# Optimization experiments

Measured on AMD Instinct MI355X. Metric: run time of the kernel, lower is better.

## Reference

```python
import jax, jax.numpy as jnp
import numpy as np
from jax.scipy.special import erfc

K, N = 64, 1024  # mixture components (n_batch), h*w for in_size=(1,32,32)


def setup_inputs() -> dict:
    key = jax.random.key(0)
    k1, k2, k3, k4, k5 = jax.random.split(key, 5)
    # Q's diagonal is the only part that survives the diagonal-matrix multiply;
    # keep it bounded away from zero so the division is well-conditioned.
    Q = jax.random.uniform(k1, (N, N), dtype=jnp.float32, minval=0.5, maxval=1.5)
    Q0 = jax.random.normal(k2, (N, 1), dtype=jnp.float32)
    base_mean = jax.random.normal(k3, (K, N), dtype=jnp.float32)
    base_var = jax.random.uniform(k4, (K, N), dtype=jnp.float32, minval=0.5, maxval=1.5)
    # mixture_probs: positive weights normalized over the component axis
    mp = jax.nn.softmax(jax.random.normal(k5, (K, N)), axis=0).astype(jnp.float32)
    mixture_probs = mp[..., None]  # [K, N, 1]
    return {"Q": Q, "Q0": Q0, "base_mean": base_mean, "base_var": base_var,
            "mixture_probs": mixture_probs, "b": 8}


def reference(Q, Q0, base_mean, base_var, mixture_probs, b):
    # Faithful math of SPNBP.compute_quant_to_alphabet.
    # The original builds dense [K,n,n] zero tensors with only the diagonal set
    # to base_mean/base_var, so Q*s2q_mean summed over the last dim reduces
    # exactly to diag(Q) * base_mean (same for the variance term).
    num_bins = 2 ** b
    qd = jnp.diagonal(Q)                               # [N]
    Qms = qd[None, :] * base_mean                      # [K, N]  == sum(Q*s2q_mean, -1)
    QQvsrt = jnp.sqrt((qd ** 2)[None, :] * base_var)   # [K, N]  == sqrt(sum(Q^2*s2q_var, -1))
    inv = 1.0 / QQvsrt[..., None]                      # [K, N, 1]
    basec = (-Qms[..., None] - Q0[None]) * inv         # [K, N, 1]
    bin_internal = jnp.arange(-num_bins // 2 + 1, num_bins // 2,
                              dtype=jnp.float32)       # [num_bins-1]
    cc = basec + bin_internal * inv                    # [K, N, num_bins-1]
    # Phi(x) = 0.5*erfc(-x/sqrt(2))  (standard normal CDF)
    Kc, Nc = base_mean.shape
    cdf = 0.5 * erfc(-cc / np.float32(np.sqrt(2.0)))
    probs = jnp.concatenate([jnp.zeros((Kc, Nc, 1), cc.dtype), cdf,
                             jnp.ones((Kc, Nc, 1), cc.dtype)], axis=-1)
    probs = probs[..., 1:] - probs[..., :-1]           # [K, N, num_bins]
    return jnp.sum(mixture_probs * probs, axis=0)      # [N, num_bins]
```

## Files before the change

kernel.cpp:

```cpp
#include <hip/hip_runtime.h>
#include <math.h>

constexpr int K  = 64;
constexpr int N  = 1024;
constexpr int NB = 256;
constexpr int NGRP = 16;
constexpr int WIN  = 16;


__device__ __forceinline__ float phi_fast(float x) {
    const float z = fabsf(x) * 0.70710678118654752f;
    const float t = __builtin_amdgcn_rcpf(fmaf(0.3275911f, z, 1.0f));
    float p = fmaf(1.061405429f, t, -1.453152027f);
    p = fmaf(p, t, 1.421413741f);
    p = fmaf(p, t, -0.284496736f);
    p = fmaf(p, t, 0.254829592f);
    p *= t;
    const float h = 0.5f * p * __expf(-z * z);
    return (x >= 0.0f) ? 1.0f - h : h;
}

__global__ __launch_bounds__(256)
void spnbp_kernel(const float* __restrict__ Q,
                  const float* __restrict__ Q0,
                  const float* __restrict__ base_mean,
                  const float* __restrict__ base_var,
                  const float* __restrict__ mp,
                  float* __restrict__ out) {
    const int n   = blockIdx.x;
    const int tid = threadIdx.x;
    const int j   = tid & (WIN - 1);
    const int grp = tid >> 4;

    __shared__ float s_mstar[K];
    __shared__ float s_inv[K];
    __shared__ float s_mp[K];
    __shared__ float s_acc[NGRP][NB];

    float* flat = &s_acc[0][0];
    #pragma unroll
    for (int r = 0; r < NGRP; ++r) flat[r * NB + tid] = 0.0f;

    if (tid < K) {
        const float qd = Q[(size_t)n * N + n];
        const float q0 = Q0[n];
        const float bm = base_mean[tid * N + n];
        const float bv = base_var[tid * N + n];
        s_inv[tid]   = 1.0f / sqrtf(qd * qd * bv);
        s_mstar[tid] = 128.0f + qd * bm + q0;
        s_mp[tid]    = mp[tid * N + n];
    }
    __syncthreads();

    #pragma unroll
    for (int i = 0; i < K / NGRP; ++i) {
        const int k       = grp * (K / NGRP) + i;
        const float mstar = s_mstar[k];
        const float inv   = s_inv[k];
        const float w     = s_mp[k];

        const int c  = (int)rintf(mstar);
        const int m0 = min(max(c - WIN / 2, 0), NB - WIN + 1);
        const int m  = m0 + j;

        float P;
        if (m == 0)       P = 0.0f;
        else if (m == NB) P = 1.0f;
        else              P = phi_fast(inv * ((float)m - mstar));

        float prev = __shfl_up(P, 1, WIN);
        if (j == 0) prev = 0.0f;

        if (m >= 1) s_acc[grp][m - 1] += w * (P - prev);
    }
    __syncthreads();

    float r = 0.0f;
    #pragma unroll
    for (int g = 0; g < NGRP; ++g) r += s_acc[g][tid];
    out[(size_t)n * NB + tid] = r;
}

extern "C" void kernel_launch(void* const* d_in, const int* in_sizes, int n_in,
                              void* d_out, int out_size, void* d_ws, size_t ws_size,
                              hipStream_t stream) {
    const float* Q         = (const float*)d_in[0];
    const float* Q0        = (const float*)d_in[1];
    const float* base_mean = (const float*)d_in[2];
    const float* base_var  = (const float*)d_in[3];
    const float* mp        = (const float*)d_in[4];
    float* out = (float*)d_out;

    spnbp_kernel<<<N, 256, 0, stream>>>(Q, Q0, base_mean, base_var, mp, out);
}
```

Before: 66.92 us.

## Split parameter prep into coalesced pre-kernel writing per-column float4 params

Adds a prep kernel that reads base_mean, base_var and mixture_probs in coalesced order and writes per-(n,k) float4 parameters, transposed so each n holds its 64 components contiguously, into the workspace. The main kernel then loads those params contiguously instead of making strided reads across K. This targets the uncoalesced gather in the original kernel but adds a second launch and a workspace round trip. The original single kernel is kept as a fallback when the workspace is too small.

```diff
diff --git a/kernel.cpp b/kernel.cpp
--- a/kernel.cpp
+++ b/kernel.cpp
@@ -21,12 +21,91 @@
 }
 
 __global__ __launch_bounds__(256)
-void spnbp_kernel(const float* __restrict__ Q,
-                  const float* __restrict__ Q0,
-                  const float* __restrict__ base_mean,
-                  const float* __restrict__ base_var,
-                  const float* __restrict__ mp,
-                  float* __restrict__ out) {
+void spnbp_prep(const float* __restrict__ Q,
+                const float* __restrict__ Q0,
+                const float* __restrict__ base_mean,
+                const float* __restrict__ base_var,
+                const float* __restrict__ mp,
+                float4* __restrict__ params) {
+    const int gid = blockIdx.x * 256 + threadIdx.x;
+    const int k   = gid >> 10;
+    const int n   = gid & (N - 1);
+
+    const float qd = Q[(size_t)n * (N + 1)];
+    const float q0 = Q0[n];
+    const float bm = base_mean[gid];
+    const float bv = base_var[gid];
+    const float w  = mp[gid];
+
+    float4 p;
+    p.x = 1.0f / sqrtf(qd * qd * bv);
+    p.y = fmaf(qd, bm, 128.0f + q0);
+    p.z = w;
+    p.w = 0.0f;
+    params[n * K + k] = p;
+}
+
+__global__ __launch_bounds__(256)
+void spnbp_main(const float4* __restrict__ params,
+                float* __restrict__ out) {
+    const int n   = blockIdx.x;
+    const int tid = threadIdx.x;
+    const int j   = tid & (WIN - 1);
+    const int grp = tid >> 4;
+
+    __shared__ float s_mstar[K];
+    __shared__ float s_inv[K];
+    __shared__ float s_mp[K];
+    __shared__ float s_acc[NGRP][NB];
+
+    float* flat = &s_acc[0][0];
+    #pragma unroll
+    for (int r = 0; r < NGRP; ++r) flat[r * NB + tid] = 0.0f;
+
+    if (tid < K) {
+        const float4 p = params[n * K + tid];
+        s_inv[tid]   = p.x;
+        s_mstar[tid] = p.y;
+        s_mp[tid]    = p.z;
+    }
+    __syncthreads();
+
+    #pragma unroll
+    for (int i = 0; i < K / NGRP; ++i) {
+        const int k       = grp * (K / NGRP) + i;
+        const float mstar = s_mstar[k];
+        const float inv   = s_inv[k];
+        const float w     = s_mp[k];
+
+        const int c  = (int)rintf(mstar);
+        const int m0 = min(max(c - WIN / 2, 0), NB - WIN + 1);
+        const int m  = m0 + j;
+
+        float P;
+        if (m == 0)       P = 0.0f;
+        else if (m == NB) P = 1.0f;
+        else              P = phi_fast(inv * ((float)m - mstar));
+
+        float prev = __shfl_up(P, 1, WIN);
+        if (j == 0) prev = 0.0f;
+
+        if (m >= 1) s_acc[grp][m - 1] += w * (P - prev);
+    }
+    __syncthreads();
+
+    float r = 0.0f;
+    #pragma unroll
+    for (int g = 0; g < NGRP; ++g) r += s_acc[g][tid];
+    out[(size_t)n * NB + tid] = r;
+}
+
+__global__ __launch_bounds__(256)
+void spnbp_mono(const float* __restrict__ Q,
+                const float* __restrict__ Q0,
+                const float* __restrict__ base_mean,
+                const float* __restrict__ base_var,
+                const float* __restrict__ mp,
+                float* __restrict__ out) {
     const int n   = blockIdx.x;
     const int tid = threadIdx.x;
     const int j   = tid & (WIN - 1);
@@ -91,5 +170,13 @@
     const float* mp        = (const float*)d_in[4];
     float* out = (float*)d_out;
 
-    spnbp_kernel<<<N, 256, 0, stream>>>(Q, Q0, base_mean, base_var, mp, out);
+    const size_t need = (size_t)N * K * sizeof(float4);
+    if (d_ws != nullptr && ws_size >= need) {
+        float4* params = (float4*)d_ws;
+        spnbp_prep<<<(K * N) / 256, 256, 0, stream>>>(Q, Q0, base_mean, base_var,
+                                                      mp, params);
+        spnbp_main<<<N, 256, 0, stream>>>(params, out);
+    } else {
+        spnbp_mono<<<N, 256, 0, stream>>>(Q, Q0, base_mean, base_var, mp, out);
+    }
 }
```

Result: slower. 68.43 us (+2.3%).
